# Optimization experiments

Measured on AMD Instinct MI355X. Metric: run time of the kernel, lower is better.

Reference implementation:

```python
import jax, jax.numpy as jnp
import numpy as np


def _conv3x3(x, w):
    # NCHW input, OIHW weight, stride 1, padding 1 (SAME for 3x3)
    return jax.lax.conv_general_dilated(
        x, w, window_strides=(1, 1), padding=((1, 1), (1, 1)),
        dimension_numbers=('NCHW', 'OIHW', 'NCHW'))


def _conv1x1(x, w):
    return jax.lax.conv_general_dilated(
        x, w, window_strides=(1, 1), padding=((0, 0), (0, 0)),
        dimension_numbers=('NCHW', 'OIHW', 'NCHW'))


def setup_inputs() -> dict:
    key = jax.random.key(0)
    k_x, k_w1, k_w2, k_wm = jax.random.split(key, 4)
    N, C, H, W = 16, 256, 64, 64
    fan = C * 9
    x = jax.random.normal(k_x, (N, C, H, W), dtype=jnp.float32)
    w1 = jax.random.normal(k_w1, (C, C, 3, 3), dtype=jnp.float32) * (2.0 / fan) ** 0.5
    w2 = jax.random.normal(k_w2, (C, C, 3, 3), dtype=jnp.float32) * (2.0 / fan) ** 0.5
    w_mask = jax.random.normal(k_wm, (1, C, 1, 1), dtype=jnp.float32) * (1.0 / C) ** 0.5
    b_mask = jnp.zeros((1,), dtype=jnp.float32)
    return {'x': x, 'w1': w1, 'w2': w2, 'w_mask': w_mask, 'b_mask': b_mask}


def reference(x, w1, w2, w_mask, b_mask):
    # MaskUnit: 1x1 conv -> logits -> hard binary mask (straight-through estimator)
    logits = _conv1x1(x, w_mask) + b_mask[None, :, None, None]  # [N,1,H,W]
    hard = (logits > 0).astype(x.dtype)
    mask = logits + jax.lax.stop_gradient(hard - logits)        # std mask, binary in fwd
    # dilated mask: 3x3 max-pool (covers 3x3 receptive field of active outputs)
    mask_dilate = jax.lax.reduce_window(
        mask, -jnp.inf, jax.lax.max, (1, 1, 3, 3), (1, 1, 1, 1), 'SAME')
    # sparse branch: conv1 gated by dilated mask, conv2 gated by std mask
    h = jax.nn.relu(_conv3x3(x, w1) * mask_dilate)
    h = jax.nn.relu(_conv3x3(h, w2) * mask)
    # apply_mask + residual (mask binary -> h*mask == h already, kept for fidelity)
    out = x + h * mask
    return out
```

## Files before the change

kernel.cpp:

```cpp
#include <hip/hip_runtime.h>
#include <hip/hip_bf16.h>

#define C_ 256
#define H_ 64
#define W_ 64
#define N_ 16
#define HW_ 4096
#define IMG_ (C_ * HW_)
#define PADIMG_ (66 * 66 * 256)
#define WT_ELEMS_ (9 * 16 * 256 * 16)

typedef short bf16x8 __attribute__((ext_vector_type(8)));
typedef float f32x16 __attribute__((ext_vector_type(16)));

__device__ __forceinline__ unsigned short f2bf(float f) {
  __hip_bfloat16 h = __float2bfloat16(f);
  return *reinterpret_cast<unsigned short*>(&h);
}

__device__ __forceinline__ void gld_lds16(const void* g, void* l) {
  __builtin_amdgcn_global_load_lds(
      (const __attribute__((address_space(1))) void*)g,
      (__attribute__((address_space(3))) void*)l, 16, 0, 0);
}

__global__ __launch_bounds__(256) void xpadmask_kernel(
    const float* __restrict__ x, const float* __restrict__ wm,
    const float* __restrict__ bm, short* __restrict__ Xp,
    unsigned char* __restrict__ mask) {
  __shared__ unsigned short lds[64 * 260];
  __shared__ float wms[256];
  __shared__ double sums[4][64];
  const int h = blockIdx.x, img = blockIdx.y;
  const int tid = threadIdx.x;
  const int wv = tid >> 6, wl = tid & 63;
  wms[tid] = wm[tid];
  __syncthreads();
  const float* xi = x + (size_t)img * IMG_ + h * 64;
  double a0 = 0.0, a1 = 0.0, a2 = 0.0, a3 = 0.0;
#pragma unroll 4
  for (int i = 0; i < 16; ++i) {
#pragma unroll
    for (int u = 0; u < 4; ++u) {
      int c = (i * 4 + u) * 4 + wv;
      float v = xi[(size_t)c * HW_ + wl];
      lds[wl * 260 + c] = f2bf(v);
      double p = (double)v * (double)wms[c];
      if (u == 0) a0 += p;
      else if (u == 1) a1 += p;
      else if (u == 2) a2 += p;
      else a3 += p;
    }
  }
  sums[wv][wl] = (a0 + a1) + (a2 + a3);
  __syncthreads();
  short* Xpimg = Xp + (size_t)img * PADIMG_;
  short* Xpi = Xpimg + ((h + 1) * 66 + 1) * 256;
#pragma unroll
  for (int j = 0; j < 16; ++j) {
    int w = j * 4 + wv;
    int c4 = wl * 4;
    uint2 d = *(const uint2*)&lds[w * 260 + c4];
    *(uint2*)&Xpi[(size_t)w * 256 + c4] = d;
  }
  if (tid < 128) {
    const int side = tid >> 6;
    const int e = (tid & 63) * 4;
    *(uint2*)&Xpimg[((size_t)(h + 1) * 66 + side * 65) * 256 + e] =
        make_uint2(0u, 0u);
  }
  if (h == 0 || h == 63) {
    uint2* rowp = (uint2*)(Xpimg + (size_t)((h == 0) ? 0 : 65) * 66 * 256);
    for (int o = tid; o < 66 * 256 / 4; o += 256) rowp[o] = make_uint2(0u, 0u);
  }
  if (wv == 0) {
    double t = sums[0][wl] + sums[1][wl] + sums[2][wl] + sums[3][wl] +
               (double)bm[0];
    mask[img * HW_ + h * 64 + wl] = (t > 0.0) ? 1 : 0;
  }
}

__global__ __launch_bounds__(256) void wt_kernel(
    const float* __restrict__ w1, const float* __restrict__ w2,
    short* __restrict__ Wt1, short* __restrict__ Wt2) {
  const int k = blockIdx.x, c = threadIdx.x;
  const float* src = blockIdx.y ? w2 : w1;
  short* dst = blockIdx.y ? Wt2 : Wt1;
  const float* s = src + ((size_t)k * 256 + c) * 9;
  const int kc = c >> 4, ce = c & 15;
#pragma unroll
  for (int t = 0; t < 9; ++t)
    dst[(((size_t)t * 16 + kc) * 256 + k) * 16 + ce] = (short)f2bf(s[t]);
}

__global__ __launch_bounds__(128) void halo_zero(short* __restrict__ Hp) {
  int p = blockIdx.x;
  int r, c;
  if (p < 66) { r = 0; c = p; }
  else if (p < 132) { r = 65; c = p - 66; }
  else if (p < 196) { r = p - 131; c = 0; }
  else { r = p - 195; c = 65; }
  unsigned int* d = (unsigned int*)(Hp + (size_t)blockIdx.y * PADIMG_ +
                                    (size_t)(r * 66 + c) * 256);
  d[threadIdx.x] = 0u;
}

#define BBUF 10560
#define WOFF 21120
#define WBUF 9216

__device__ __forceinline__ void stage_BW(short* sm, int buf, const short* Xb,
                                         const short* Wg, int ch0, int kc,
                                         int wave, int lane) {
  short* Bd = sm + buf * BBUF;
  short* Wd = sm + WOFF + buf * WBUF;
  const int ko = kc * 16;
#pragma unroll
  for (int q = 0; q < 10; ++q) {
    const int n = wave + 4 * q;
    if (n < 22) {
      const int h = (n >= 11) ? 1 : 0;
      const int i = n - h * 11;
      const int row0 = (i < 10) ? i * 64 : 596;
      gld_lds16(Xb + (size_t)(row0 + lane) * 256 + ko + h * 8,
                Bd + h * 5280 + row0 * 8);
    } else {
      const int m = n - 22;
      const int t = m >> 1, ih = m & 1;
      gld_lds16(Wg + (((size_t)t * 16 + kc) * 256 + ch0 + ih * 32 +
                      (lane & 31)) * 16 + (lane >> 5) * 8,
                Wd + (t * 2 + ih) * 512);
    }
  }
}

template <int EPI>
__global__ __launch_bounds__(256, 2) void conv_mfma(
    const short* __restrict__ src, const short* __restrict__ Wt,
    const unsigned char* __restrict__ gate, const float* __restrict__ xres,
    short* __restrict__ dstH, float* __restrict__ dstF, int swz) {
  __shared__ __align__(16) short sm[2 * BBUF + 2 * WBUF];

  const int tid = threadIdx.x;
  const int lane = tid & 63, wave = tid >> 6;
  const int ln31 = lane & 31, kh = lane >> 5;

  int bx, by, bz;
  {
    int d = blockIdx.x + 4 * (blockIdx.y + 8 * blockIdx.z);
    if (swz) {
      int k = d & 7, j = d >> 3;
      bx = j & 3;
      by = (j >> 2) & 7;
      bz = ((j >> 5) << 3) + k;
    } else {
      bx = blockIdx.x;
      by = blockIdx.y;
      bz = blockIdx.z;
    }
  }
  const int ch0 = bx * 64;
  const int h0 = by * 8;
  const int img = bz;

  const short* Xb = src + (size_t)img * PADIMG_ + (size_t)(h0 * 66) * 256;

  f32x16 acc[2][4];
#pragma unroll
  for (int i = 0; i < 2; ++i)
#pragma unroll
    for (int j = 0; j < 4; ++j)
#pragma unroll
      for (int e = 0; e < 16; ++e) acc[i][j][e] = 0.f;

  stage_BW(sm, 0, Xb, Wt, ch0, 0, wave, lane);
  asm volatile("s_waitcnt vmcnt(0)\n\ts_barrier" ::: "memory");

  for (int kk = 0; kk < 16; ++kk) {
    const int cur = kk & 1;
    if (kk < 15) stage_BW(sm, cur ^ 1, Xb, Wt, ch0, kk + 1, wave, lane);

    const short* Bth = sm + cur * BBUF + kh * 5280 + (wave * 132 + ln31) * 8;
    const short* Wth = sm + WOFF + cur * WBUF + (kh * 32 + ln31) * 8;

    bf16x8 ac[2], bc[4], an[2], bn[4];
#pragma unroll
    for (int i = 0; i < 2; ++i)
      ac[i] = *(const bf16x8*)(Wth + i * 512);
#pragma unroll
    for (int j = 0; j < 4; ++j)
      bc[j] = *(const bf16x8*)(Bth + ((j >> 1) * 66 + (j & 1) * 32) * 8);

#pragma unroll
    for (int t = 0; t < 9; ++t) {
      if (t < 8) {
        const int dy = (t + 1) / 3, dx = (t + 1) % 3;
#pragma unroll
        for (int i = 0; i < 2; ++i)
          an[i] = *(const bf16x8*)(Wth + ((t + 1) * 2 + i) * 512);
#pragma unroll
        for (int j = 0; j < 4; ++j)
          bn[j] = *(const bf16x8*)(Bth +
                                   (((j >> 1) + dy) * 66 + (j & 1) * 32 + dx) * 8);
      }
      __builtin_amdgcn_s_setprio(1);
#pragma unroll
      for (int j = 0; j < 4; ++j) {
        acc[0][j] = __builtin_amdgcn_mfma_f32_32x32x16_bf16(ac[0], bc[j],
                                                            acc[0][j], 0, 0, 0);
        acc[1][j] = __builtin_amdgcn_mfma_f32_32x32x16_bf16(ac[1], bc[j],
                                                            acc[1][j], 0, 0, 0);
      }
      __builtin_amdgcn_s_setprio(0);
      if (t < 8) {
#pragma unroll
        for (int i = 0; i < 2; ++i) ac[i] = an[i];
#pragma unroll
        for (int j = 0; j < 4; ++j) bc[j] = bn[j];
      }
    }
    if (kk < 15)
      asm volatile("s_waitcnt vmcnt(0)\n\ts_barrier" ::: "memory");
  }

  const int rb = h0 + wave * 2;
#pragma unroll
  for (int j = 0; j < 4; ++j) {
    const int r = rb + (j >> 1);
    const int col = (j & 1) * 32 + ln31;
    const int pidx = r * 64 + col;
    unsigned int g;
    if (EPI == 0) {
      g = 0;
#pragma unroll
      for (int dy = -1; dy <= 1; ++dy) {
        const int rr = r + dy;
        if (rr < 0 || rr >= H_) continue;
#pragma unroll
        for (int dx = -1; dx <= 1; ++dx) {
          const int cc = col + dx;
          if (cc < 0 || cc >= W_) continue;
          g |= gate[img * HW_ + rr * W_ + cc];
        }
      }
    } else {
      g = gate[img * HW_ + pidx];
    }
#pragma unroll
    for (int i = 0; i < 2; ++i) {
      const f32x16 v = acc[i][j];
#pragma unroll
      for (int rg = 0; rg < 4; ++rg) {
        const int ch = ch0 + i * 32 + rg * 8 + kh * 4;
        float e0 = g ? fmaxf(v[rg * 4 + 0], 0.f) : 0.f;
        float e1 = g ? fmaxf(v[rg * 4 + 1], 0.f) : 0.f;
        float e2 = g ? fmaxf(v[rg * 4 + 2], 0.f) : 0.f;
        float e3 = g ? fmaxf(v[rg * 4 + 3], 0.f) : 0.f;
        if (EPI == 0) {
          uint2 u;
          u.x = (unsigned int)f2bf(e0) | ((unsigned int)f2bf(e1) << 16);
          u.y = (unsigned int)f2bf(e2) | ((unsigned int)f2bf(e3) << 16);
          short* dp = dstH + (size_t)img * PADIMG_ +
                      ((size_t)((r + 1) * 66 + (col + 1))) * 256 + ch;
          *(uint2*)dp = u;
        } else {
          size_t o = (size_t)img * IMG_ + (size_t)ch * HW_ + pidx;
          dstF[o] = xres[o] + e0;
          dstF[o + HW_] = xres[o + HW_] + e1;
          dstF[o + 2 * HW_] = xres[o + 2 * HW_] + e2;
          dstF[o + 3 * HW_] = xres[o + 3 * HW_] + e3;
        }
      }
    }
  }
}

extern "C" void kernel_launch(void* const* d_in, const int* in_sizes, int n_in,
                              void* d_out, int out_size, void* d_ws,
                              size_t ws_size, hipStream_t stream) {
  const float* x = (const float*)d_in[0];
  const float* w1 = (const float*)d_in[1];
  const float* w2 = (const float*)d_in[2];
  const float* wmask = (const float*)d_in[3];
  const float* bmask = (const float*)d_in[4];
  float* out = (float*)d_out;

  char* ws = (char*)d_ws;
  unsigned char* mask = (unsigned char*)ws;
  short* Wt1 = (short*)(ws + 65536);
  short* Wt2 = Wt1 + WT_ELEMS_;
  const size_t fixed = 65536 + 4 * (size_t)WT_ELEMS_;
  short* Xp = (short*)(ws + fixed);

  const size_t tailpad = 32768;
  const size_t per_img = 2 * (size_t)PADIMG_ * 2;
  int B = (ws_size > fixed + tailpad)
              ? (int)((ws_size - fixed - tailpad) / per_img) : 0;
  if (B > N_) B = N_;
  if (B < 1) B = 1;
  short* Hp = Xp + (size_t)B * PADIMG_;

  wt_kernel<<<dim3(256, 2), 256, 0, stream>>>(w1, w2, Wt1, Wt2);
  halo_zero<<<dim3(260, B), 128, 0, stream>>>(Hp);

  for (int n0 = 0; n0 < N_; n0 += B) {
    const int nb = (N_ - n0 < B) ? (N_ - n0) : B;
    const int swz = (nb % 8 == 0) ? 1 : 0;
    xpadmask_kernel<<<dim3(64, nb), 256, 0, stream>>>(
        x + (size_t)n0 * IMG_, wmask, bmask, Xp, mask + n0 * HW_);
    conv_mfma<0><<<dim3(4, 8, nb), 256, 0, stream>>>(
        Xp, Wt1, mask + n0 * HW_, nullptr, Hp, nullptr, swz);
    conv_mfma<1><<<dim3(4, 8, nb), 256, 0, stream>>>(
        Hp, Wt2, mask + n0 * HW_, x + (size_t)n0 * IMG_, nullptr,
        out + (size_t)n0 * IMG_, swz);
  }
}
```

Measured before the change: 287.2 us.

## Stagger conv tap order per wave, vectorize mask prep, merge setup kernels

Each wave in the conv kernel now starts its 9-tap loop at a different tap, so the four waves read different LDS rows at the same moment and are meant to hit fewer bank conflicts. The four template instantiations enlarge the code and add a branch on the wave index. The mask/pad kernel now reads x with float4 loads and reduces the 1x1 mask logits over 16 channel groups. The weight-transpose and halo-zero kernels are merged into one launch to save launch overhead.

Result: slower. 754.2 us (+162.6%).

```diff
diff --git a/kernel.cpp b/kernel.cpp
--- a/kernel.cpp
+++ b/kernel.cpp
@@ -29,33 +29,38 @@
     const float* __restrict__ bm, short* __restrict__ Xp,
     unsigned char* __restrict__ mask) {
   __shared__ unsigned short lds[64 * 260];
+  __shared__ double dsum[16][64];
   __shared__ float wms[256];
-  __shared__ double sums[4][64];
   const int h = blockIdx.x, img = blockIdx.y;
   const int tid = threadIdx.x;
-  const int wv = tid >> 6, wl = tid & 63;
+  const int pxq = tid & 15, cg = tid >> 4;
+  const int p0 = pxq * 4;
   wms[tid] = wm[tid];
   __syncthreads();
   const float* xi = x + (size_t)img * IMG_ + h * 64;
-  double a0 = 0.0, a1 = 0.0, a2 = 0.0, a3 = 0.0;
-#pragma unroll 4
+  double s0 = 0.0, s1 = 0.0, s2 = 0.0, s3 = 0.0;
+#pragma unroll
   for (int i = 0; i < 16; ++i) {
-#pragma unroll
-    for (int u = 0; u < 4; ++u) {
-      int c = (i * 4 + u) * 4 + wv;
-      float v = xi[(size_t)c * HW_ + wl];
-      lds[wl * 260 + c] = f2bf(v);
-      double p = (double)v * (double)wms[c];
-      if (u == 0) a0 += p;
-      else if (u == 1) a1 += p;
-      else if (u == 2) a2 += p;
-      else a3 += p;
-    }
-  }
-  sums[wv][wl] = (a0 + a1) + (a2 + a3);
+    const int c = cg * 16 + i;
+    const float4 v = *(const float4*)&xi[(size_t)c * HW_ + p0];
+    lds[(p0 + 0) * 260 + c] = f2bf(v.x);
+    lds[(p0 + 1) * 260 + c] = f2bf(v.y);
+    lds[(p0 + 2) * 260 + c] = f2bf(v.z);
+    lds[(p0 + 3) * 260 + c] = f2bf(v.w);
+    const double wmc = (double)wms[c];
+    s0 += (double)v.x * wmc;
+    s1 += (double)v.y * wmc;
+    s2 += (double)v.z * wmc;
+    s3 += (double)v.w * wmc;
+  }
+  dsum[cg][p0 + 0] = s0;
+  dsum[cg][p0 + 1] = s1;
+  dsum[cg][p0 + 2] = s2;
+  dsum[cg][p0 + 3] = s3;
   __syncthreads();
   short* Xpimg = Xp + (size_t)img * PADIMG_;
   short* Xpi = Xpimg + ((h + 1) * 66 + 1) * 256;
+  const int wv = tid >> 6, wl = tid & 63;
 #pragma unroll
   for (int j = 0; j < 16; ++j) {
     int w = j * 4 + wv;
@@ -73,36 +78,43 @@
     uint2* rowp = (uint2*)(Xpimg + (size_t)((h == 0) ? 0 : 65) * 66 * 256);
     for (int o = tid; o < 66 * 256 / 4; o += 256) rowp[o] = make_uint2(0u, 0u);
   }
-  if (wv == 0) {
-    double t = sums[0][wl] + sums[1][wl] + sums[2][wl] + sums[3][wl] +
-               (double)bm[0];
-    mask[img * HW_ + h * 64 + wl] = (t > 0.0) ? 1 : 0;
-  }
-}
-
-__global__ __launch_bounds__(256) void wt_kernel(
+  if (tid < 64) {
+    double t = (double)bm[0];
+#pragma unroll
+    for (int g = 0; g < 16; ++g) t += dsum[g][tid];
+    mask[img * HW_ + h * 64 + tid] = (t > 0.0) ? 1 : 0;
+  }
+}
+
+__global__ __launch_bounds__(256) void wt_halo_kernel(
     const float* __restrict__ w1, const float* __restrict__ w2,
-    short* __restrict__ Wt1, short* __restrict__ Wt2) {
-  const int k = blockIdx.x, c = threadIdx.x;
-  const float* src = blockIdx.y ? w2 : w1;
-  short* dst = blockIdx.y ? Wt2 : Wt1;
-  const float* s = src + ((size_t)k * 256 + c) * 9;
-  const int kc = c >> 4, ce = c & 15;
-#pragma unroll
-  for (int t = 0; t < 9; ++t)
-    dst[(((size_t)t * 16 + kc) * 256 + k) * 16 + ce] = (short)f2bf(s[t]);
-}
-
-__global__ __launch_bounds__(128) void halo_zero(short* __restrict__ Hp) {
-  int p = blockIdx.x;
-  int r, c;
-  if (p < 66) { r = 0; c = p; }
-  else if (p < 132) { r = 65; c = p - 66; }
-  else if (p < 196) { r = p - 131; c = 0; }
-  else { r = p - 195; c = 65; }
-  unsigned int* d = (unsigned int*)(Hp + (size_t)blockIdx.y * PADIMG_ +
-                                    (size_t)(r * 66 + c) * 256);
-  d[threadIdx.x] = 0u;
+    short* __restrict__ Wt1, short* __restrict__ Wt2,
+    short* __restrict__ Hp) {
+  const int bx = blockIdx.x;
+  const int tid = threadIdx.x;
+  if (bx < 512) {
+    const int k = bx & 255, which = bx >> 8;
+    const float* src = which ? w2 : w1;
+    short* dst = which ? Wt2 : Wt1;
+    const float* s = src + ((size_t)k * 256 + tid) * 9;
+    const int kc = tid >> 4, ce = tid & 15;
+#pragma unroll
+    for (int t = 0; t < 9; ++t)
+      dst[(((size_t)t * 16 + kc) * 256 + k) * 16 + ce] = (short)f2bf(s[t]);
+  } else {
+    const int img = bx - 512;
+    short* Hpi = Hp + (size_t)img * PADIMG_;
+    for (int q = tid; q < 260 * 32; q += 256) {
+      const int p = q >> 5, seg = q & 31;
+      int r, c;
+      if (p < 66) { r = 0; c = p; }
+      else if (p < 132) { r = 65; c = p - 66; }
+      else if (p < 196) { r = p - 131; c = 0; }
+      else { r = p - 195; c = 65; }
+      uint4* d = (uint4*)(Hpi + (size_t)(r * 66 + c) * 256);
+      d[seg] = make_uint4(0u, 0u, 0u, 0u);
+    }
+  }
 }
 
 #define BBUF 10560
@@ -134,6 +146,50 @@
   }
 }
 
+template <int R>
+__device__ __forceinline__ void do_taps(const short* Bth, const short* Wth,
+                                        f32x16 (&acc)[2][4]) {
+  bf16x8 ac[2], bc[4], an[2], bn[4];
+  {
+    constexpr int t0 = R % 9;
+    constexpr int dy = t0 / 3, dx = t0 % 3;
+    ac[0] = *(const bf16x8*)(Wth + (t0 * 2 + 0) * 512);
+    ac[1] = *(const bf16x8*)(Wth + (t0 * 2 + 1) * 512);
+#pragma unroll
+    for (int j = 0; j < 4; ++j)
+      bc[j] = *(const bf16x8*)(Bth +
+                               (((j >> 1) + dy) * 66 + (j & 1) * 32 + dx) * 8);
+  }
+#pragma unroll
+  for (int u = 0; u < 9; ++u) {
+    if (u < 8) {
+      const int t = (R + u + 1) % 9;
+      const int dy = t / 3, dx = t % 3;
+      an[0] = *(const bf16x8*)(Wth + (t * 2 + 0) * 512);
+      an[1] = *(const bf16x8*)(Wth + (t * 2 + 1) * 512);
+#pragma unroll
+      for (int j = 0; j < 4; ++j)
+        bn[j] = *(const bf16x8*)(Bth +
+                                 (((j >> 1) + dy) * 66 + (j & 1) * 32 + dx) * 8);
+    }
+    __builtin_amdgcn_s_setprio(1);
+#pragma unroll
+    for (int j = 0; j < 4; ++j) {
+      acc[0][j] = __builtin_amdgcn_mfma_f32_32x32x16_bf16(ac[0], bc[j],
+                                                          acc[0][j], 0, 0, 0);
+      acc[1][j] = __builtin_amdgcn_mfma_f32_32x32x16_bf16(ac[1], bc[j],
+                                                          acc[1][j], 0, 0, 0);
+    }
+    __builtin_amdgcn_s_setprio(0);
+    if (u < 8) {
+#pragma unroll
+      for (int i = 0; i < 2; ++i) ac[i] = an[i];
+#pragma unroll
+      for (int j = 0; j < 4; ++j) bc[j] = bn[j];
+    }
+  }
+}
+
 template <int EPI>
 __global__ __launch_bounds__(256, 2) void conv_mfma(
     const short* __restrict__ src, const short* __restrict__ Wt,
@@ -183,42 +239,11 @@
     const short* Bth = sm + cur * BBUF + kh * 5280 + (wave * 132 + ln31) * 8;
     const short* Wth = sm + WOFF + cur * WBUF + (kh * 32 + ln31) * 8;
 
-    bf16x8 ac[2], bc[4], an[2], bn[4];
-#pragma unroll
-    for (int i = 0; i < 2; ++i)
-      ac[i] = *(const bf16x8*)(Wth + i * 512);
-#pragma unroll
-    for (int j = 0; j < 4; ++j)
-      bc[j] = *(const bf16x8*)(Bth + ((j >> 1) * 66 + (j & 1) * 32) * 8);
-
-#pragma unroll
-    for (int t = 0; t < 9; ++t) {
-      if (t < 8) {
-        const int dy = (t + 1) / 3, dx = (t + 1) % 3;
-#pragma unroll
-        for (int i = 0; i < 2; ++i)
-          an[i] = *(const bf16x8*)(Wth + ((t + 1) * 2 + i) * 512);
-#pragma unroll
-        for (int j = 0; j < 4; ++j)
-          bn[j] = *(const bf16x8*)(Bth +
-                                   (((j >> 1) + dy) * 66 + (j & 1) * 32 + dx) * 8);
-      }
-      __builtin_amdgcn_s_setprio(1);
-#pragma unroll
-      for (int j = 0; j < 4; ++j) {
-        acc[0][j] = __builtin_amdgcn_mfma_f32_32x32x16_bf16(ac[0], bc[j],
-                                                            acc[0][j], 0, 0, 0);
-        acc[1][j] = __builtin_amdgcn_mfma_f32_32x32x16_bf16(ac[1], bc[j],
-                                                            acc[1][j], 0, 0, 0);
-      }
-      __builtin_amdgcn_s_setprio(0);
-      if (t < 8) {
-#pragma unroll
-        for (int i = 0; i < 2; ++i) ac[i] = an[i];
-#pragma unroll
-        for (int j = 0; j < 4; ++j) bc[j] = bn[j];
-      }
-    }
+    if (wave == 0) do_taps<0>(Bth, Wth, acc);
+    else if (wave == 1) do_taps<2>(Bth, Wth, acc);
+    else if (wave == 2) do_taps<4>(Bth, Wth, acc);
+    else do_taps<6>(Bth, Wth, acc);
+
     if (kk < 15)
       asm volatile("s_waitcnt vmcnt(0)\n\ts_barrier" ::: "memory");
   }
@@ -300,8 +325,7 @@
   if (B < 1) B = 1;
   short* Hp = Xp + (size_t)B * PADIMG_;
 
-  wt_kernel<<<dim3(256, 2), 256, 0, stream>>>(w1, w2, Wt1, Wt2);
-  halo_zero<<<dim3(260, B), 128, 0, stream>>>(Hp);
+  wt_halo_kernel<<<512 + B, 256, 0, stream>>>(w1, w2, Wt1, Wt2, Hp);
 
   for (int n0 = 0; n0 < N_; n0 += B) {
     const int nb = (N_ - n0 < B) ? (N_ - n0) : B;
```
